# Kernel optimization log

Measured on AMD Instinct MI355X. Metric: run time of the kernel, lower is better.

Reference implementation:

```python
import jax, jax.numpy as jnp
import numpy as np

H = 768
R = 24


def setup_inputs() -> dict:
    key = jax.random.key(0)
    ks = jax.random.split(key, 9)
    B, S = 4, 256
    hidden = jax.random.normal(ks[0], (B, S, H), dtype=jnp.float32)
    # ConcatHandshaking fc: Linear(2H -> H); torch weight shape (out,in)=(H,2H)
    fc_w = jax.random.normal(ks[1], (H, 2 * H), dtype=jnp.float32) * (1.0 / np.sqrt(2 * H))
    fc_b = jnp.zeros((H,), dtype=jnp.float32)
    # h2t: Linear(H -> 2)
    h2t_w = jax.random.normal(ks[2], (2, H), dtype=jnp.float32) * (1.0 / np.sqrt(H))
    h2t_b = jnp.zeros((2,), dtype=jnp.float32)
    # h2h / t2t TaggingProjector: R independent Linear(H -> 3), batched as (R,3,H)
    h2h_w = jax.random.normal(ks[3], (R, 3, H), dtype=jnp.float32) * (1.0 / np.sqrt(H))
    h2h_b = jnp.zeros((R, 3), dtype=jnp.float32)
    t2t_w = jax.random.normal(ks[4], (R, 3, H), dtype=jnp.float32) * (1.0 / np.sqrt(H))
    t2t_b = jnp.zeros((R, 3), dtype=jnp.float32)
    return {
        "hidden": hidden,
        "fc_w": fc_w, "fc_b": fc_b,
        "h2t_w": h2t_w, "h2t_b": h2t_b,
        "h2h_w": h2h_w, "h2h_b": h2h_b,
        "t2t_w": t2t_w, "t2t_b": t2t_b,
    }


def _handshaking(hidden, fc_w, fc_b):
    # hidden: (B, S, H). Pairs (i, j) with i <= j in row-major (torch loop) order.
    S = hidden.shape[1]
    idx_i, idx_j = jnp.triu_indices(S)  # each (P,), P = S(S+1)/2
    # concat([h_i, h_j]) @ W^T == h_i @ Wl^T + h_j @ Wr^T  (avoids (B,P,2H) buffer)
    Wl = fc_w[:, :H]  # (H, H)
    Wr = fc_w[:, H:]  # (H, H)
    left = jnp.einsum('bsh,oh->bso', hidden, Wl)   # (B, S, H)
    right = jnp.einsum('bsh,oh->bso', hidden, Wr)  # (B, S, H)
    hs = jnp.tanh(left[:, idx_i, :] + right[:, idx_j, :] + fc_b)  # (B, P, H)
    return hs


def reference(hidden, fc_w, fc_b, h2t_w, h2t_b, h2h_w, h2h_b, t2t_w, t2t_b):
    hs = _handshaking(hidden, fc_w, fc_b)  # (B, P, H)
    # h2t: plain Linear(H->2), logits (no softmax in original)
    h2t = jnp.einsum('bph,oh->bpo', hs, h2t_w) + h2t_b  # (B, P, 2)
    # TaggingProjector: batched per-relation Linear(H->3), then softmax over tags
    h2h = jax.nn.softmax(jnp.einsum('bph,rth->brpt', hs, h2h_w) + h2h_b[None, :, None, :], axis=-1)
    t2t = jax.nn.softmax(jnp.einsum('bph,rth->brpt', hs, t2t_w) + t2t_b[None, :, None, :], axis=-1)
    return (h2t, h2h, t2t)
```

## Files before the change

### kernel.cpp

```cpp
#include <hip/hip_runtime.h>
#include <hip/hip_bf16.h>

#define H 768
#define SEQ 256
#define NPAIR 32896
#define NTOT 131584
#define NOUTP 160
#define OFF_H2H 263168u
#define OFF_T2T 9737216u

#define N_BPK 122880
#define N_FCW 1179648
#define SCL 2.8853900817779268f

#define CH 64
#define NCH 12
#define BSLOT 24576
#define SLAB_STR 166

typedef short bf16x8 __attribute__((ext_vector_type(8)));
typedef float f32x4 __attribute__((ext_vector_type(4)));

__device__ __forceinline__ float tanh_s(float xs) {
    float e = __builtin_amdgcn_exp2f(xs);
    return fmaf(-2.0f, __builtin_amdgcn_rcpf(e + 1.0f), 1.0f);
}
__device__ __forceinline__ float bf_lo(int w){ return __uint_as_float(((unsigned)w) << 16); }
__device__ __forceinline__ float bf_hi(int w){ return __uint_as_float(((unsigned)w) & 0xffff0000u); }
__device__ __forceinline__ float bfu(unsigned short u){ return __uint_as_float(((unsigned)u) << 16); }
__device__ __forceinline__ int cvtpk(float lo, float hi) {
    int r;
    asm("v_cvt_pk_bf16_f32 %0, %1, %2" : "=v"(r) : "v"(lo), "v"(hi));
    return r;
}
__device__ __forceinline__ unsigned short bf16r(float x){
    unsigned int u = __float_as_uint(x);
    u += 0x7fffu + ((u >> 16) & 1u);
    return (unsigned short)(u >> 16);
}
__device__ __forceinline__ bf16x8 tanh_frag(int4 lv, int4 rv) {
    int4 st;
    st.x = cvtpk(tanh_s(bf_lo(lv.x) + bf_lo(rv.x)), tanh_s(bf_hi(lv.x) + bf_hi(rv.x)));
    st.y = cvtpk(tanh_s(bf_lo(lv.y) + bf_lo(rv.y)), tanh_s(bf_hi(lv.y) + bf_hi(rv.y)));
    st.z = cvtpk(tanh_s(bf_lo(lv.z) + bf_lo(rv.z)), tanh_s(bf_hi(lv.z) + bf_hi(rv.z)));
    st.w = cvtpk(tanh_s(bf_lo(lv.w) + bf_lo(rv.w)), tanh_s(bf_hi(lv.w) + bf_hi(rv.w)));
    return __builtin_bit_cast(bf16x8, st);
}

typedef const __attribute__((address_space(1))) unsigned int* as1_u32p;
typedef __attribute__((address_space(3))) unsigned int* as3_u32p;
__device__ __forceinline__ void gload_lds16(const void* g, void* l) {
    __builtin_amdgcn_global_load_lds((as1_u32p)g, (as3_u32p)l, 16, 0, 0);
}

__device__ __forceinline__ int row_start(int i) { return i * SEQ - (i * (i - 1)) / 2; }
__device__ __forceinline__ void pair_ij(int p, int& oi, int& oj) {
    double disc = 263169.0 - 8.0 * (double)p;
    int i = (int)((513.0 - sqrt(disc)) * 0.5);
    if (i > 0 && row_start(i) > p) --i;
    while (row_start(i + 1) <= p) ++i;
    oi = i;
    oj = i + (p - row_start(i));
}
__device__ __forceinline__ int batch_of(int g) {
    return (g >= 3 * NPAIR) ? 3 : (g >= 2 * NPAIR) ? 2 : (g >= NPAIR) ? 1 : 0;
}

__global__ __launch_bounds__(256) void pack_kernel(
    const float* __restrict__ h2t_w, const float* __restrict__ h2h_w,
    const float* __restrict__ t2t_w, const float* __restrict__ h2t_b,
    const float* __restrict__ h2h_b, const float* __restrict__ t2t_b,
    const float* __restrict__ fc_w,
    unsigned short* __restrict__ Bpk, unsigned short* __restrict__ fcwb,
    float* __restrict__ bc)
{
    int idx = blockIdx.x * 256 + threadIdx.x;
    if (idx < N_BPK) {
        int j = idx & 7, lane = (idx >> 3) & 63, rest = idx >> 9;
        int frag = rest % 20, c = rest / 20;
        int f = frag % 10, kk = frag / 10;
        int n = f * 16 + (lane & 15);
        int k = c * CH + kk * 32 + ((lane >> 4) << 3) + j;
        float v = 0.f;
        if (n < 2)        v = h2t_w[n * H + k];
        else if (n < 74)  v = h2h_w[(n - 2) * H + k];
        else if (n < 146) v = t2t_w[(n - 74) * H + k];
        Bpk[c * 12288 + (idx - c * 10240)] = bf16r(v);
    } else if (idx < N_BPK + N_FCW) {
        int q = idx - N_BPK;
        int n = q / H, k = q % H;
        float v = (n < H) ? fc_w[(size_t)n * 2 * H + k]
                          : fc_w[(size_t)(n - H) * 2 * H + H + k];
        fcwb[q] = bf16r(v);
    } else if (idx < N_BPK + N_FCW + NOUTP) {
        int q = idx - N_BPK - N_FCW;
        float v = 0.f;
        if (q < 2)        v = h2t_b[q];
        else if (q < 74)  v = h2h_b[q - 2];
        else if (q < 146) v = t2t_b[q - 74];
        bc[q] = v;
    }
}

__global__ __launch_bounds__(256, 2) void lr_mfma(
    const float* __restrict__ hidden, const unsigned short* __restrict__ fcwb,
    const float* __restrict__ fc_b,
    unsigned short* __restrict__ LB, unsigned short* __restrict__ RB)
{
    __shared__ __align__(16) char sm[16384];
    const int tid = threadIdx.x, l = tid & 63, w = tid >> 6;
    const int wm = w >> 1, wn = w & 1;
    const int m0 = blockIdx.x * 64, n0 = blockIdx.y * 64;
    f32x4 acc[2][2] = {};
    for (int c = 0; c < 12; ++c) {
        const int k0 = c * 64;
        #pragma unroll
        for (int it = 0; it < 2; ++it) {
            int idx = tid + it * 256;
            int row = idx >> 3, k8 = idx & 7;
            const float4* src = reinterpret_cast<const float4*>(hidden + (size_t)(m0 + row) * H + k0 + k8 * 8);
            float4 a = src[0], bq = src[1];
            int4 st;
            st.x = cvtpk(a.x, a.y);  st.y = cvtpk(a.z, a.w);
            st.z = cvtpk(bq.x, bq.y); st.w = cvtpk(bq.z, bq.w);
            *reinterpret_cast<int4*>(sm + row * 128 + ((k8 * 16) ^ ((row & 7) << 4))) = st;
        }
        #pragma unroll
        for (int it = 0; it < 2; ++it) {
            int idx = tid + it * 256;
            int row = idx >> 3, k8 = idx & 7;
            *reinterpret_cast<int4*>(sm + 8192 + row * 128 + ((k8 * 16) ^ ((row & 7) << 4))) =
                *reinterpret_cast<const int4*>(fcwb + (size_t)(n0 + row) * H + k0 + k8 * 8);
        }
        __syncthreads();
        #pragma unroll
        for (int kk = 0; kk < 2; ++kk) {
            const int sl = kk * 4 + (l >> 4);
            const int swz = (l & 7) << 4;
            bf16x8 af[2], bfr[2];
            #pragma unroll
            for (int a = 0; a < 2; ++a) {
                int row = 32 * wm + 16 * a + (l & 15);
                af[a] = *reinterpret_cast<const bf16x8*>(sm + row * 128 + ((sl * 16) ^ swz));
            }
            #pragma unroll
            for (int f = 0; f < 2; ++f) {
                int row = 32 * wn + 16 * f + (l & 15);
                bfr[f] = *reinterpret_cast<const bf16x8*>(sm + 8192 + row * 128 + ((sl * 16) ^ swz));
            }
            #pragma unroll
            for (int a = 0; a < 2; ++a)
                #pragma unroll
                for (int f = 0; f < 2; ++f)
                    acc[a][f] = __builtin_amdgcn_mfma_f32_16x16x32_bf16(af[a], bfr[f], acc[a][f], 0, 0, 0);
        }
        __syncthreads();
    }
    #pragma unroll
    for (int a = 0; a < 2; ++a)
        #pragma unroll
        for (int f = 0; f < 2; ++f)
            #pragma unroll
            for (int r = 0; r < 4; ++r) {
                int row = m0 + 32 * wm + 16 * a + 4 * (l >> 4) + r;
                int col = n0 + 32 * wn + 16 * f + (l & 15);
                float v = acc[a][f][r];
                if (n0 < H) LB[(size_t)row * H + col] = bf16r((v + fc_b[col]) * SCL);
                else        RB[(size_t)row * H + (col - H)] = bf16r(v * SCL);
            }
}

__global__ __launch_bounds__(512, 2) void pair_mfma(
    const unsigned short* __restrict__ LB, const unsigned short* __restrict__ RB,
    const unsigned short* __restrict__ Bpk, const float* __restrict__ bc,
    float* __restrict__ out)
{
    __shared__ __align__(16) char sm[49792];
    float* bc_s = reinterpret_cast<float*>(sm + 49152);

    const int tid = threadIdx.x, l = tid & 63, w = tid >> 6;
    const int g0 = blockIdx.x * 128;
    const int b = batch_of(g0);
    const int p0 = g0 - b * NPAIR;

    if (tid < NOUTP) bc_s[tid] = bc[tid];

    const int row = 16 * w + (l & 15);
    int pi, pj;
    pair_ij(p0 + row, pi, pj);
    const int kb = (l >> 4) << 3;
    const unsigned short* lp = LB + (size_t)(b * SEQ + pi) * H + kb;
    const unsigned short* rp = RB + (size_t)(b * SEQ + pj) * H + kb;

    const char* bpk = reinterpret_cast<const char*>(Bpk);
    const int soff = tid * 16;
    const int doff = w * 1024;

    f32x4 acc[10] = {};

    {
        gload_lds16(bpk + soff,          sm + doff);
        gload_lds16(bpk + soff + 8192,   sm + doff + 8192);
        gload_lds16(bpk + soff + 16384,  sm + doff + 16384);
        __builtin_amdgcn_sched_barrier(0);
    }
    int4 lv0 = *reinterpret_cast<const int4*>(lp);
    int4 lv1 = *reinterpret_cast<const int4*>(lp + 32);
    int4 rv0 = *reinterpret_cast<const int4*>(rp);
    int4 rv1 = *reinterpret_cast<const int4*>(rp + 32);
    asm volatile("s_waitcnt vmcnt(4) lgkmcnt(0)" ::: "memory");
    __builtin_amdgcn_s_barrier();
    __builtin_amdgcn_sched_barrier(0);

    #pragma unroll 2
    for (int c = 0; c < NCH - 1; ++c) {
        char* bufn = sm + (((c + 1) & 1) ? BSLOT : 0);
        const char* bn = bpk + (c + 1) * BSLOT + soff;
        gload_lds16(bn,          bufn + doff);
        gload_lds16(bn + 8192,   bufn + doff + 8192);
        gload_lds16(bn + 16384,  bufn + doff + 16384);
        __builtin_amdgcn_sched_barrier(0);
        bf16x8 a0 = tanh_frag(lv0, rv0);
        bf16x8 a1 = tanh_frag(lv1, rv1);
        const int co = (c + 1) * CH;
        lv0 = *reinterpret_cast<const int4*>(lp + co);
        lv1 = *reinterpret_cast<const int4*>(lp + co + 32);
        rv0 = *reinterpret_cast<const int4*>(rp + co);
        rv1 = *reinterpret_cast<const int4*>(rp + co + 32);
        const char* bufc = sm + ((c & 1) ? BSLOT : 0);
        #pragma unroll
        for (int f = 0; f < 10; ++f) {
            bf16x8 bfr = *reinterpret_cast<const bf16x8*>(bufc + (f * 64 + l) * 16);
            acc[f] = __builtin_amdgcn_mfma_f32_16x16x32_bf16(a0, bfr, acc[f], 0, 0, 0);
        }
        #pragma unroll
        for (int f = 0; f < 10; ++f) {
            bf16x8 bfr = *reinterpret_cast<const bf16x8*>(bufc + ((10 + f) * 64 + l) * 16);
            acc[f] = __builtin_amdgcn_mfma_f32_16x16x32_bf16(a1, bfr, acc[f], 0, 0, 0);
        }
        asm volatile("s_waitcnt vmcnt(4) lgkmcnt(0)" ::: "memory");
        __builtin_amdgcn_s_barrier();
        __builtin_amdgcn_sched_barrier(0);
    }
    {
        bf16x8 a0 = tanh_frag(lv0, rv0);
        bf16x8 a1 = tanh_frag(lv1, rv1);
        const char* bufc = sm + BSLOT;
        #pragma unroll
        for (int f = 0; f < 10; ++f) {
            bf16x8 bfr = *reinterpret_cast<const bf16x8*>(bufc + (f * 64 + l) * 16);
            acc[f] = __builtin_amdgcn_mfma_f32_16x16x32_bf16(a0, bfr, acc[f], 0, 0, 0);
        }
        #pragma unroll
        for (int f = 0; f < 10; ++f) {
            bf16x8 bfr = *reinterpret_cast<const bf16x8*>(bufc + ((10 + f) * 64 + l) * 16);
            acc[f] = __builtin_amdgcn_mfma_f32_16x16x32_bf16(a1, bfr, acc[f], 0, 0, 0);
        }
    }
    asm volatile("s_waitcnt lgkmcnt(0)" ::: "memory");
    __builtin_amdgcn_s_barrier();

    unsigned short* slab = reinterpret_cast<unsigned short*>(sm);
    #pragma unroll
    for (int f = 0; f < 10; ++f)
        #pragma unroll
        for (int r = 0; r < 4; ++r) {
            int rw = 16 * w + 4 * (l >> 4) + r;
            slab[rw * SLAB_STR + f * 16 + (l & 15)] = bf16r(acc[f][r]);
        }
    __syncthreads();

    if (tid < 256) {
        int pr = tid >> 1, tt = tid & 1;
        float val = bfu(slab[pr * SLAB_STR + tt]) + bc_s[tt];
        __builtin_nontemporal_store(val, &out[(size_t)(g0 + pr) * 2 + tt]);
    }
    #pragma unroll
    for (int it = 0; it < 12; ++it) {
        int item = it * 512 + tid;
        int pr = item & 127, rr = item >> 7;
        int p = p0 + pr;
        int ob = 2 + rr * 3;
        const unsigned short* sp = slab + pr * SLAB_STR + ob;
        float l0 = bfu(sp[0]) + bc_s[ob + 0];
        float l1 = bfu(sp[1]) + bc_s[ob + 1];
        float l2 = bfu(sp[2]) + bc_s[ob + 2];
        float mx = fmaxf(l0, fmaxf(l1, l2));
        float e0 = __expf(l0 - mx), e1 = __expf(l1 - mx), e2 = __expf(l2 - mx);
        float inv = __fdividef(1.0f, e0 + e1 + e2);
        size_t base = (rr < 24)
            ? (size_t)OFF_H2H + ((size_t)(b * 24 + rr) * NPAIR + p) * 3
            : (size_t)OFF_T2T + ((size_t)(b * 24 + rr - 24) * NPAIR + p) * 3;
        __builtin_nontemporal_store(e0 * inv, &out[base + 0]);
        __builtin_nontemporal_store(e1 * inv, &out[base + 1]);
        __builtin_nontemporal_store(e2 * inv, &out[base + 2]);
    }
}

extern "C" void kernel_launch(void* const* d_in, const int* in_sizes, int n_in,
                              void* d_out, int out_size, void* d_ws, size_t ws_size,
                              hipStream_t stream) {
    const float* hidden = (const float*)d_in[0];
    const float* fc_w   = (const float*)d_in[1];
    const float* fc_b   = (const float*)d_in[2];
    const float* h2t_w  = (const float*)d_in[3];
    const float* h2t_b  = (const float*)d_in[4];
    const float* h2h_w  = (const float*)d_in[5];
    const float* h2h_b  = (const float*)d_in[6];
    const float* t2t_w  = (const float*)d_in[7];
    const float* t2t_b  = (const float*)d_in[8];

    char* wsb = (char*)d_ws;
    unsigned short* LBw  = (unsigned short*)(wsb);
    unsigned short* RBw  = (unsigned short*)(wsb + 1572864);
    unsigned short* Bpk  = (unsigned short*)(wsb + 3145728);
    unsigned short* fcwb = (unsigned short*)(wsb + 3440640);
    float*          bc   = (float*)        (wsb + 5799936);

    float* out = (float*)d_out;

    pack_kernel<<<(N_BPK + N_FCW + NOUTP + 255) / 256, 256, 0, stream>>>(
        h2t_w, h2h_w, t2t_w, h2t_b, h2h_b, t2t_b, fc_w, Bpk, fcwb, bc);
    lr_mfma<<<dim3(16, 24), 256, 0, stream>>>(hidden, fcwb, fc_b, LBw, RBw);
    pair_mfma<<<NTOT / 128, 512, 0, stream>>>(LBw, RBw, Bpk, bc, out);
}
```

Before: 98.95 us.

## Switch pair kernel to 32x32 MFMA tiles and fuse fc_w bf16 conversion

The pair kernel now runs 256 threads per block. Each wave computes 32 pair rows using 32x32x16 bf16 MFMAs into five 16-wide accumulators, instead of 16-row tiles with ten 16x16x32 MFMAs per wave. The projection weights are repacked to match the new fragment layout, and the epilogue runs twice as many softmax iterations per thread. Separately, the fc_w bf16 pre-conversion pass is removed and lr_mfma converts fp32 weights on the fly, which saves a kernel-sized write and read but doubles the weight bytes loaded per tile. The larger MFMA tile cuts LDS fragment reads per FLOP, at the cost of more registers per thread and fewer threads per block.

Measured after the change: 95.75 us. -3.2%, faster.

```diff
diff --git a/kernel.cpp b/kernel.cpp
--- a/kernel.cpp
+++ b/kernel.cpp
@@ -10,7 +10,6 @@
 #define OFF_T2T 9737216u
 
 #define N_BPK 122880
-#define N_FCW 1179648
 #define SCL 2.8853900817779268f
 
 #define CH 64
@@ -20,6 +19,7 @@
 
 typedef short bf16x8 __attribute__((ext_vector_type(8)));
 typedef float f32x4 __attribute__((ext_vector_type(4)));
+typedef float f32x16 __attribute__((ext_vector_type(16)));
 
 __device__ __forceinline__ float tanh_s(float xs) {
     float e = __builtin_amdgcn_exp2f(xs);
@@ -70,30 +70,22 @@
     const float* __restrict__ h2t_w, const float* __restrict__ h2h_w,
     const float* __restrict__ t2t_w, const float* __restrict__ h2t_b,
     const float* __restrict__ h2h_b, const float* __restrict__ t2t_b,
-    const float* __restrict__ fc_w,
-    unsigned short* __restrict__ Bpk, unsigned short* __restrict__ fcwb,
-    float* __restrict__ bc)
+    unsigned short* __restrict__ Bpk, float* __restrict__ bc)
 {
     int idx = blockIdx.x * 256 + threadIdx.x;
     if (idx < N_BPK) {
         int j = idx & 7, lane = (idx >> 3) & 63, rest = idx >> 9;
-        int frag = rest % 20, c = rest / 20;
-        int f = frag % 10, kk = frag / 10;
-        int n = f * 16 + (lane & 15);
-        int k = c * CH + kk * 32 + ((lane >> 4) << 3) + j;
+        int fr = rest % 20, c = rest / 20;
+        int s = fr / 5, f = fr % 5;
+        int n = f * 32 + (lane & 31);
+        int k = c * CH + s * 16 + ((lane >> 5) << 3) + j;
         float v = 0.f;
         if (n < 2)        v = h2t_w[n * H + k];
         else if (n < 74)  v = h2h_w[(n - 2) * H + k];
         else if (n < 146) v = t2t_w[(n - 74) * H + k];
         Bpk[c * 12288 + (idx - c * 10240)] = bf16r(v);
-    } else if (idx < N_BPK + N_FCW) {
+    } else if (idx < N_BPK + NOUTP) {
         int q = idx - N_BPK;
-        int n = q / H, k = q % H;
-        float v = (n < H) ? fc_w[(size_t)n * 2 * H + k]
-                          : fc_w[(size_t)(n - H) * 2 * H + H + k];
-        fcwb[q] = bf16r(v);
-    } else if (idx < N_BPK + N_FCW + NOUTP) {
-        int q = idx - N_BPK - N_FCW;
         float v = 0.f;
         if (q < 2)        v = h2t_b[q];
         else if (q < 74)  v = h2h_b[q - 2];
@@ -103,7 +95,7 @@
 }
 
 __global__ __launch_bounds__(256, 2) void lr_mfma(
-    const float* __restrict__ hidden, const unsigned short* __restrict__ fcwb,
+    const float* __restrict__ hidden, const float* __restrict__ fc_w,
     const float* __restrict__ fc_b,
     unsigned short* __restrict__ LB, unsigned short* __restrict__ RB)
 {
@@ -129,8 +121,15 @@
         for (int it = 0; it < 2; ++it) {
             int idx = tid + it * 256;
             int row = idx >> 3, k8 = idx & 7;
-            *reinterpret_cast<int4*>(sm + 8192 + row * 128 + ((k8 * 16) ^ ((row & 7) << 4))) =
-                *reinterpret_cast<const int4*>(fcwb + (size_t)(n0 + row) * H + k0 + k8 * 8);
+            const float* fsrc = (n0 < H)
+                ? fc_w + (size_t)(n0 + row) * (2 * H) + k0 + k8 * 8
+                : fc_w + (size_t)(n0 - H + row) * (2 * H) + H + k0 + k8 * 8;
+            const float4* src = reinterpret_cast<const float4*>(fsrc);
+            float4 a = src[0], bq = src[1];
+            int4 st;
+            st.x = cvtpk(a.x, a.y);  st.y = cvtpk(a.z, a.w);
+            st.z = cvtpk(bq.x, bq.y); st.w = cvtpk(bq.z, bq.w);
+            *reinterpret_cast<int4*>(sm + 8192 + row * 128 + ((k8 * 16) ^ ((row & 7) << 4))) = st;
         }
         __syncthreads();
         #pragma unroll
@@ -170,7 +169,7 @@
             }
 }
 
-__global__ __launch_bounds__(512, 2) void pair_mfma(
+__global__ __launch_bounds__(256) void pair_mfma(
     const unsigned short* __restrict__ LB, const unsigned short* __restrict__ RB,
     const unsigned short* __restrict__ Bpk, const float* __restrict__ bc,
     float* __restrict__ out)
@@ -185,76 +184,108 @@
 
     if (tid < NOUTP) bc_s[tid] = bc[tid];
 
-    const int row = 16 * w + (l & 15);
+    const int row = 32 * w + (l & 31);
     int pi, pj;
     pair_ij(p0 + row, pi, pj);
-    const int kb = (l >> 4) << 3;
+    const int kb = (l >> 5) << 3;
     const unsigned short* lp = LB + (size_t)(b * SEQ + pi) * H + kb;
     const unsigned short* rp = RB + (size_t)(b * SEQ + pj) * H + kb;
 
     const char* bpk = reinterpret_cast<const char*>(Bpk);
-    const int soff = tid * 16;
+    const int soff = w * 1024 + l * 16;
     const int doff = w * 1024;
 
-    f32x4 acc[10] = {};
+    f32x16 acc[5] = {};
 
     {
-        gload_lds16(bpk + soff,          sm + doff);
-        gload_lds16(bpk + soff + 8192,   sm + doff + 8192);
-        gload_lds16(bpk + soff + 16384,  sm + doff + 16384);
+        #pragma unroll
+        for (int r = 0; r < 5; ++r)
+            gload_lds16(bpk + r * 4096 + soff, sm + r * 4096 + doff);
         __builtin_amdgcn_sched_barrier(0);
     }
     int4 lv0 = *reinterpret_cast<const int4*>(lp);
-    int4 lv1 = *reinterpret_cast<const int4*>(lp + 32);
+    int4 lv1 = *reinterpret_cast<const int4*>(lp + 16);
+    int4 lv2 = *reinterpret_cast<const int4*>(lp + 32);
+    int4 lv3 = *reinterpret_cast<const int4*>(lp + 48);
     int4 rv0 = *reinterpret_cast<const int4*>(rp);
-    int4 rv1 = *reinterpret_cast<const int4*>(rp + 32);
-    asm volatile("s_waitcnt vmcnt(4) lgkmcnt(0)" ::: "memory");
+    int4 rv1 = *reinterpret_cast<const int4*>(rp + 16);
+    int4 rv2 = *reinterpret_cast<const int4*>(rp + 32);
+    int4 rv3 = *reinterpret_cast<const int4*>(rp + 48);
+    asm volatile("s_waitcnt vmcnt(8) lgkmcnt(0)" ::: "memory");
     __builtin_amdgcn_s_barrier();
     __builtin_amdgcn_sched_barrier(0);
 
     #pragma unroll 2
     for (int c = 0; c < NCH - 1; ++c) {
         char* bufn = sm + (((c + 1) & 1) ? BSLOT : 0);
-        const char* bn = bpk + (c + 1) * BSLOT + soff;
-        gload_lds16(bn,          bufn + doff);
-        gload_lds16(bn + 8192,   bufn + doff + 8192);
-        gload_lds16(bn + 16384,  bufn + doff + 16384);
+        const char* bn = bpk + (c + 1) * BSLOT;
+        #pragma unroll
+        for (int r = 0; r < 5; ++r)
+            gload_lds16(bn + r * 4096 + soff, bufn + r * 4096 + doff);
         __builtin_amdgcn_sched_barrier(0);
         bf16x8 a0 = tanh_frag(lv0, rv0);
         bf16x8 a1 = tanh_frag(lv1, rv1);
+        bf16x8 a2 = tanh_frag(lv2, rv2);
+        bf16x8 a3 = tanh_frag(lv3, rv3);
         const int co = (c + 1) * CH;
         lv0 = *reinterpret_cast<const int4*>(lp + co);
-        lv1 = *reinterpret_cast<const int4*>(lp + co + 32);
+        lv1 = *reinterpret_cast<const int4*>(lp + co + 16);
+        lv2 = *reinterpret_cast<const int4*>(lp + co + 32);
+        lv3 = *reinterpret_cast<const int4*>(lp + co + 48);
         rv0 = *reinterpret_cast<const int4*>(rp + co);
-        rv1 = *reinterpret_cast<const int4*>(rp + co + 32);
+        rv1 = *reinterpret_cast<const int4*>(rp + co + 16);
+        rv2 = *reinterpret_cast<const int4*>(rp + co + 32);
+        rv3 = *reinterpret_cast<const int4*>(rp + co + 48);
         const char* bufc = sm + ((c & 1) ? BSLOT : 0);
         #pragma unroll
-        for (int f = 0; f < 10; ++f) {
-            bf16x8 bfr = *reinterpret_cast<const bf16x8*>(bufc + (f * 64 + l) * 16);
-            acc[f] = __builtin_amdgcn_mfma_f32_16x16x32_bf16(a0, bfr, acc[f], 0, 0, 0);
-        }
-        #pragma unroll
-        for (int f = 0; f < 10; ++f) {
-            bf16x8 bfr = *reinterpret_cast<const bf16x8*>(bufc + ((10 + f) * 64 + l) * 16);
-            acc[f] = __builtin_amdgcn_mfma_f32_16x16x32_bf16(a1, bfr, acc[f], 0, 0, 0);
-        }
-        asm volatile("s_waitcnt vmcnt(4) lgkmcnt(0)" ::: "memory");
+        for (int f = 0; f < 5; ++f) {
+            bf16x8 bfr = *reinterpret_cast<const bf16x8*>(bufc + ((0 * 5 + f) * 64 + l) * 16);
+            acc[f] = __builtin_amdgcn_mfma_f32_32x32x16_bf16(a0, bfr, acc[f], 0, 0, 0);
+        }
+        #pragma unroll
+        for (int f = 0; f < 5; ++f) {
+            bf16x8 bfr = *reinterpret_cast<const bf16x8*>(bufc + ((1 * 5 + f) * 64 + l) * 16);
+            acc[f] = __builtin_amdgcn_mfma_f32_32x32x16_bf16(a1, bfr, acc[f], 0, 0, 0);
+        }
+        #pragma unroll
+        for (int f = 0; f < 5; ++f) {
+            bf16x8 bfr = *reinterpret_cast<const bf16x8*>(bufc + ((2 * 5 + f) * 64 + l) * 16);
+            acc[f] = __builtin_amdgcn_mfma_f32_32x32x16_bf16(a2, bfr, acc[f], 0, 0, 0);
+        }
+        #pragma unroll
+        for (int f = 0; f < 5; ++f) {
+            bf16x8 bfr = *reinterpret_cast<const bf16x8*>(bufc + ((3 * 5 + f) * 64 + l) * 16);
+            acc[f] = __builtin_amdgcn_mfma_f32_32x32x16_bf16(a3, bfr, acc[f], 0, 0, 0);
+        }
+        asm volatile("s_waitcnt vmcnt(8) lgkmcnt(0)" ::: "memory");
         __builtin_amdgcn_s_barrier();
         __builtin_amdgcn_sched_barrier(0);
     }
     {
         bf16x8 a0 = tanh_frag(lv0, rv0);
         bf16x8 a1 = tanh_frag(lv1, rv1);
+        bf16x8 a2 = tanh_frag(lv2, rv2);
+        bf16x8 a3 = tanh_frag(lv3, rv3);
         const char* bufc = sm + BSLOT;
         #pragma unroll
-        for (int f = 0; f < 10; ++f) {
-            bf16x8 bfr = *reinterpret_cast<const bf16x8*>(bufc + (f * 64 + l) * 16);
-            acc[f] = __builtin_amdgcn_mfma_f32_16x16x32_bf16(a0, bfr, acc[f], 0, 0, 0);
-        }
-        #pragma unroll
-        for (int f = 0; f < 10; ++f) {
-            bf16x8 bfr = *reinterpret_cast<const bf16x8*>(bufc + ((10 + f) * 64 + l) * 16);
-            acc[f] = __builtin_amdgcn_mfma_f32_16x16x32_bf16(a1, bfr, acc[f], 0, 0, 0);
+        for (int f = 0; f < 5; ++f) {
+            bf16x8 bfr = *reinterpret_cast<const bf16x8*>(bufc + ((0 * 5 + f) * 64 + l) * 16);
+            acc[f] = __builtin_amdgcn_mfma_f32_32x32x16_bf16(a0, bfr, acc[f], 0, 0, 0);
+        }
+        #pragma unroll
+        for (int f = 0; f < 5; ++f) {
+            bf16x8 bfr = *reinterpret_cast<const bf16x8*>(bufc + ((1 * 5 + f) * 64 + l) * 16);
+            acc[f] = __builtin_amdgcn_mfma_f32_32x32x16_bf16(a1, bfr, acc[f], 0, 0, 0);
+        }
+        #pragma unroll
+        for (int f = 0; f < 5; ++f) {
+            bf16x8 bfr = *reinterpret_cast<const bf16x8*>(bufc + ((2 * 5 + f) * 64 + l) * 16);
+            acc[f] = __builtin_amdgcn_mfma_f32_32x32x16_bf16(a2, bfr, acc[f], 0, 0, 0);
+        }
+        #pragma unroll
+        for (int f = 0; f < 5; ++f) {
+            bf16x8 bfr = *reinterpret_cast<const bf16x8*>(bufc + ((3 * 5 + f) * 64 + l) * 16);
+            acc[f] = __builtin_amdgcn_mfma_f32_32x32x16_bf16(a3, bfr, acc[f], 0, 0, 0);
         }
     }
     asm volatile("s_waitcnt lgkmcnt(0)" ::: "memory");
@@ -262,22 +293,22 @@
 
     unsigned short* slab = reinterpret_cast<unsigned short*>(sm);
     #pragma unroll
-    for (int f = 0; f < 10; ++f)
-        #pragma unroll
-        for (int r = 0; r < 4; ++r) {
-            int rw = 16 * w + 4 * (l >> 4) + r;
-            slab[rw * SLAB_STR + f * 16 + (l & 15)] = bf16r(acc[f][r]);
+    for (int f = 0; f < 5; ++f)
+        #pragma unroll
+        for (int g = 0; g < 16; ++g) {
+            int rw = 32 * w + (g & 3) + 8 * (g >> 2) + 4 * (l >> 5);
+            slab[rw * SLAB_STR + f * 32 + (l & 31)] = bf16r(acc[f][g]);
         }
     __syncthreads();
 
-    if (tid < 256) {
+    {
         int pr = tid >> 1, tt = tid & 1;
         float val = bfu(slab[pr * SLAB_STR + tt]) + bc_s[tt];
         __builtin_nontemporal_store(val, &out[(size_t)(g0 + pr) * 2 + tt]);
     }
     #pragma unroll
-    for (int it = 0; it < 12; ++it) {
-        int item = it * 512 + tid;
+    for (int it = 0; it < 24; ++it) {
+        int item = it * 256 + tid;
         int pr = item & 127, rr = item >> 7;
         int p = p0 + pr;
         int ob = 2 + rr * 3;
@@ -314,13 +345,12 @@
     unsigned short* LBw  = (unsigned short*)(wsb);
     unsigned short* RBw  = (unsigned short*)(wsb + 1572864);
     unsigned short* Bpk  = (unsigned short*)(wsb + 3145728);
-    unsigned short* fcwb = (unsigned short*)(wsb + 3440640);
-    float*          bc   = (float*)        (wsb + 5799936);
+    float*          bc   = (float*)        (wsb + 3440640);
 
     float* out = (float*)d_out;
 
-    pack_kernel<<<(N_BPK + N_FCW + NOUTP + 255) / 256, 256, 0, stream>>>(
-        h2t_w, h2h_w, t2t_w, h2t_b, h2h_b, t2t_b, fc_w, Bpk, fcwb, bc);
-    lr_mfma<<<dim3(16, 24), 256, 0, stream>>>(hidden, fcwb, fc_b, LBw, RBw);
-    pair_mfma<<<NTOT / 128, 512, 0, stream>>>(LBw, RBw, Bpk, bc, out);
-}
+    pack_kernel<<<(N_BPK + NOUTP + 255) / 256, 256, 0, stream>>>(
+        h2t_w, h2h_w, t2t_w, h2t_b, h2h_b, t2t_b, Bpk, bc);
+    lr_mfma<<<dim3(16, 24), 256, 0, stream>>>(hidden, fc_w, fc_b, LBw, RBw);
+    pair_mfma<<<NTOT / 128, 256, 0, stream>>>(LBw, RBw, Bpk, bc, out);
+}
```
